# Kernel optimization log

Hardware: AMD Instinct MI355X
Metric: run time of the kernel (lower is better)

Reference implementation:

```python
import jax, jax.numpy as jnp
import numpy as np

N, D, K = 262144, 64, 1024


def setup_inputs() -> dict:
    key = jax.random.key(0)
    kx, kc = jax.random.split(key)
    x = jax.random.normal(kx, (N, D), dtype=jnp.float32)
    codebook = jax.random.normal(kc, (K, D), dtype=jnp.float32)
    return {"x": x, "codebook": codebook}


def reference(x, codebook):
    # VQTokenizer.encode: cdist(x, codebook) -> argmin -> gather.
    # squared distances equals argmin over cdist (sqrt is monotone).
    x2 = jnp.sum(x * x, axis=-1, keepdims=True)            # (N, 1)
    c2 = jnp.sum(codebook * codebook, axis=-1)             # (K,)
    d2 = x2 + c2[None, :] - 2.0 * jnp.einsum('nd,kd->nk', x, codebook)  # (N, K)
    encoded = jnp.argmin(d2, axis=1)                       # (N,) int
    quantized = jnp.take(codebook, encoded, axis=0)        # (N, D)
    return encoded, quantized
```

## Files before the change

### kernel.cpp

```cpp
#include <hip/hip_runtime.h>
#include <hip/hip_bf16.h>

#define NPTS 262144
#define DDIM 64
#define KCB  1024
#define CHUNK 128
#define NCHUNK (KCB / CHUNK)
#define GPC (CHUNK / 16)

typedef __attribute__((ext_vector_type(8))) short short8;
typedef __attribute__((ext_vector_type(4))) float f32x4;

static __device__ __forceinline__ unsigned short f2bf_rne(float f) {
    union { float f; unsigned u; } v; v.f = f;
    unsigned r = v.u + 0x7FFFu + ((v.u >> 16) & 1u);
    return (unsigned short)(r >> 16);
}
static __device__ __forceinline__ float bf2f(unsigned short h) {
    union { unsigned u; float f; } v; v.u = ((unsigned)h) << 16;
    return v.f;
}
static __device__ __forceinline__ bool beats(float sa, int ka, float sb, int kb) {
    return (sa > sb) || (sa == sb && ka < kb);
}

__global__ __launch_bounds__(256) void c2n_kernel(const float* __restrict__ cb,
                                                  float* __restrict__ c2n) {
    int k = blockIdx.x * blockDim.x + threadIdx.x;
    if (k >= KCB) return;
    const float4* row = (const float4*)(cb + (size_t)k * DDIM);
    float s0 = 0.f, s1 = 0.f, s2 = 0.f, s3 = 0.f;
#pragma unroll
    for (int j = 0; j < DDIM / 4; ++j) {
        float4 a = row[j];
        s0 = __builtin_fmaf(a.x, a.x, s0);
        s1 = __builtin_fmaf(a.y, a.y, s1);
        s2 = __builtin_fmaf(a.z, a.z, s2);
        s3 = __builtin_fmaf(a.w, a.w, s3);
    }
    c2n[k] = 256.0f - 0.5f * ((s0 + s1) + (s2 + s3));
}

__global__ __launch_bounds__(256) void pack_kernel(const float* __restrict__ cb,
                                                   unsigned short* __restrict__ G) {
    int t = blockIdx.x * 256 + threadIdx.x;
    int r = t >> 3, d8 = t & 7;
    const float4* src = (const float4*)(cb + (size_t)r * DDIM + d8 * 8);
    float4 v0 = src[0], v1 = src[1];
    float vv[8] = {v0.x, v0.y, v0.z, v0.w, v1.x, v1.y, v1.z, v1.w};
    short8 h, l;
#pragma unroll
    for (int j = 0; j < 8; ++j) {
        unsigned short hb = f2bf_rne(vv[j]);
        h[j] = (short)hb;
        l[j] = (short)f2bf_rne(vv[j] - bf2f(hb));
    }
    int c = r >> 7, g = (r >> 4) & 7, col = r & 15;
    int ks = d8 >> 2, q = d8 & 3;
    size_t base = (size_t)c * 16384 + g * 1024 + ks * 512 + q * 128 + col * 8;
    *(short8*)(G + base) = h;
    *(short8*)(G + base + 8192) = l;
}

__global__ __launch_bounds__(256, 2) void vq_main(const float* __restrict__ x,
                                                  const float* __restrict__ cb,
                                                  const float* __restrict__ c2n,
                                                  const unsigned short* __restrict__ G,
                                                  float* __restrict__ out) {
    __shared__ unsigned short frag[2][CHUNK * DDIM * 2];
    __shared__ int lds_bk1[256];
    __shared__ int lds_bk2[256];

    const int tid = threadIdx.x;
    const int lane = tid & 63;
    const int wave = tid >> 6;
    const int b15 = lane & 15;
    const int q = lane >> 4;
    const int blk_base = blockIdx.x * 256;
    const int wave_base = blk_base + wave * 64;
    const int lane_off = lane * 16;

    short8 Ahi[4][2], Alo[4][2];
#pragma unroll
    for (int t = 0; t < 4; ++t) {
        const float* xr = x + (size_t)(wave_base + t * 16 + b15) * DDIM + q * 8;
#pragma unroll
        for (int ks = 0; ks < 2; ++ks) {
            float4 v0 = *(const float4*)(xr + ks * 32);
            float4 v1 = *(const float4*)(xr + ks * 32 + 4);
            float vv[8] = {v0.x, v0.y, v0.z, v0.w, v1.x, v1.y, v1.z, v1.w};
            short8 h, l;
#pragma unroll
            for (int j = 0; j < 8; ++j) {
                unsigned short hb = f2bf_rne(vv[j]);
                h[j] = (short)hb;
                l[j] = (short)f2bf_rne(vv[j] - bf2f(hb));
            }
            Ahi[t][ks] = h;
            Alo[t][ks] = l;
        }
    }

    unsigned int b1[16], b2[16];
#pragma unroll
    for (int i = 0; i < 16; ++i) { b1[i] = 0u; b2[i] = 0u; }

#define STAGE(cc, buf)                                                                     \
    {                                                                                      \
        const unsigned char* gsrc =                                                        \
            (const unsigned char*)G + (size_t)(cc) * 32768 + wave * 1024 + lane * 16;      \
        unsigned char* ldst = (unsigned char*)&frag[buf][0] + wave * 1024;                 \
        _Pragma("unroll") for (int it = 0; it < 8; ++it)                                   \
            __builtin_amdgcn_global_load_lds(                                              \
                (const __attribute__((address_space(1))) unsigned int*)(gsrc + it * 4096), \
                (__attribute__((address_space(3))) unsigned int*)(ldst + it * 4096),       \
                16, 0, 0);                                                                 \
    }

    float c2v[GPC], c2vn[GPC];
    STAGE(0, 0);
#pragma unroll
    for (int g = 0; g < GPC; ++g) c2v[g] = c2n[g * 16 + b15];
    __syncthreads();

    for (int c = 0; c < NCHUNK; ++c) {
        const int cur = c & 1;
        if (c + 1 < NCHUNK) {
            STAGE(c + 1, cur ^ 1);
#pragma unroll
            for (int g = 0; g < GPC; ++g) c2vn[g] = c2n[(c + 1) * CHUNK + g * 16 + b15];
        }
        const unsigned char* fb = (const unsigned char*)&frag[cur][0];

#pragma unroll
        for (int g = 0; g < GPC; ++g) {
            f32x4 acc[4];
#pragma unroll
            for (int t = 0; t < 4; ++t) acc[t] = (f32x4){c2v[g], c2v[g], c2v[g], c2v[g]};
            __builtin_amdgcn_s_setprio(1);
#pragma unroll
            for (int ks = 0; ks < 2; ++ks) {
                const short8 Bhi = *(const short8*)(fb + g * 2048 + ks * 1024 + lane_off);
                const short8 Blo = *(const short8*)(fb + 16384 + g * 2048 + ks * 1024 + lane_off);
#pragma unroll
                for (int t = 0; t < 4; ++t) {
                    acc[t] = __builtin_amdgcn_mfma_f32_16x16x32_bf16(Ahi[t][ks], Bhi, acc[t], 0, 0, 0);
                    acc[t] = __builtin_amdgcn_mfma_f32_16x16x32_bf16(Ahi[t][ks], Blo, acc[t], 0, 0, 0);
                    acc[t] = __builtin_amdgcn_mfma_f32_16x16x32_bf16(Alo[t][ks], Bhi, acc[t], 0, 0, 0);
                }
            }
            __builtin_amdgcn_s_setprio(0);
            const unsigned int inv = 63u - (unsigned)(c * GPC + g);
#pragma unroll
            for (int t = 0; t < 4; ++t) {
#pragma unroll
                for (int r = 0; r < 4; ++r) {
                    int i = t * 4 + r;
                    unsigned int kb = (__float_as_uint(acc[t][r]) & 0xFFFFFFC0u) | inv;
                    unsigned int mn = b1[i] < kb ? b1[i] : kb;
                    b1[i] = b1[i] > kb ? b1[i] : kb;
                    b2[i] = b2[i] > mn ? b2[i] : mn;
                }
            }
        }
#pragma unroll
        for (int g = 0; g < GPC; ++g) c2v[g] = c2vn[g];
        __syncthreads();
    }
#undef STAGE

    unsigned int K1[16], K2[16];
    int I1[16], I2[16];
#pragma unroll
    for (int i = 0; i < 16; ++i) {
        K1[i] = b1[i]; I1[i] = (int)(63u - (b1[i] & 63u)) * 16 + b15;
        K2[i] = b2[i]; I2[i] = (int)(63u - (b2[i] & 63u)) * 16 + b15;
    }
#pragma unroll
    for (int m = 1; m < 16; m <<= 1) {
#pragma unroll
        for (int i = 0; i < 16; ++i) {
            unsigned int o1 = __shfl_xor(K1[i], m); int oi1 = __shfl_xor(I1[i], m);
            unsigned int o2 = __shfl_xor(K2[i], m); int oi2 = __shfl_xor(I2[i], m);
            bool ob = (o1 > K1[i]) || (o1 == K1[i] && oi1 < I1[i]);
            unsigned int nk1, nk2; int ni1, ni2;
            if (ob) {
                nk1 = o1; ni1 = oi1;
                bool sb = (K1[i] > o2) || (K1[i] == o2 && I1[i] < oi2);
                nk2 = sb ? K1[i] : o2; ni2 = sb ? I1[i] : oi2;
            } else {
                nk1 = K1[i]; ni1 = I1[i];
                bool sb = (o1 > K2[i]) || (o1 == K2[i] && oi1 < I2[i]);
                nk2 = sb ? o1 : K2[i]; ni2 = sb ? oi1 : I2[i];
            }
            K1[i] = nk1; I1[i] = ni1; K2[i] = nk2; I2[i] = ni2;
        }
    }

    if (b15 == 0) {
#pragma unroll
        for (int t = 0; t < 4; ++t)
#pragma unroll
            for (int r = 0; r < 4; ++r) {
                int pl = wave * 64 + t * 16 + q * 4 + r;
                lds_bk1[pl] = I1[t * 4 + r];
                lds_bk2[pl] = I2[t * 4 + r];
            }
    }
    __syncthreads();

    const int p = blk_base + tid;
    const int k1 = lds_bk1[tid], k2 = lds_bk2[tid];
    const float4* xr = (const float4*)(x + (size_t)p * DDIM);
    const float4* c1 = (const float4*)(cb + (size_t)k1 * DDIM);
    const float4* c2r = (const float4*)(cb + (size_t)k2 * DDIM);
    float d1a = 0.f, d1b = 0.f, d2a = 0.f, d2b = 0.f;
#pragma unroll
    for (int j = 0; j < 16; ++j) {
        float4 xv = xr[j];
        float4 u = c1[j], w = c2r[j];
        d1a = __builtin_fmaf(xv.x, u.x, d1a); d1b = __builtin_fmaf(xv.y, u.y, d1b);
        d1a = __builtin_fmaf(xv.z, u.z, d1a); d1b = __builtin_fmaf(xv.w, u.w, d1b);
        d2a = __builtin_fmaf(xv.x, w.x, d2a); d2b = __builtin_fmaf(xv.y, w.y, d2b);
        d2a = __builtin_fmaf(xv.z, w.z, d2a); d2b = __builtin_fmaf(xv.w, w.w, d2b);
    }
    float a1 = (d1a + d1b) + c2n[k1];
    float a2 = (d2a + d2b) + c2n[k2];
    int kf = beats(a1, k1, a2, k2) ? k1 : k2;

    out[p] = (float)kf;
    const float4* cf = (const float4*)(cb + (size_t)kf * DDIM);
    float4* qo = (float4*)(out + NPTS + (size_t)p * DDIM);
#pragma unroll
    for (int j = 0; j < 16; ++j) qo[j] = cf[j];
}

extern "C" void kernel_launch(void* const* d_in, const int* in_sizes, int n_in,
                              void* d_out, int out_size, void* d_ws, size_t ws_size,
                              hipStream_t stream) {
    const float* x = (const float*)d_in[0];
    const float* cb = (const float*)d_in[1];
    float* c2n = (float*)d_ws;
    unsigned short* G = (unsigned short*)((char*)d_ws + 4096);

    hipLaunchKernelGGL(c2n_kernel, dim3(KCB / 256), dim3(256), 0, stream, cb, c2n);
    hipLaunchKernelGGL(pack_kernel, dim3(KCB * 8 / 256), dim3(256), 0, stream, cb, G);
    hipLaunchKernelGGL(vq_main, dim3(NPTS / 256), dim3(256), 0, stream,
                       x, cb, c2n, G, (float*)d_out);
}
```

Baseline: 163.0 us.

## Use 512-thread blocks with 32 points per wave and smaller codebook chunks

Blocks grow to 8 waves, and each wave now handles 32 points instead of 64. The codebook chunk shrinks to 64 entries, which cuts LDS use and register pressure so occupancy can rise (launch bounds 512,4). The top-2 tracking now processes two groups at once using float max3/med3 on packed keys. The final refine and gather step is split across two threads per point, with a shuffle to pick the winner. In exchange, each loaded codebook chunk is reused over fewer points, so MFMA work per LDS load drops, and there are more chunk iterations and more syncs.

```diff
diff --git a/kernel.cpp b/kernel.cpp
--- a/kernel.cpp
+++ b/kernel.cpp
@@ -4,9 +4,10 @@
 #define NPTS 262144
 #define DDIM 64
 #define KCB  1024
-#define CHUNK 128
+#define CHUNK 64
 #define NCHUNK (KCB / CHUNK)
 #define GPC (CHUNK / 16)
+#define PPB 256
 
 typedef __attribute__((ext_vector_type(8))) short short8;
 typedef __attribute__((ext_vector_type(4))) float f32x4;
@@ -22,6 +23,9 @@
 }
 static __device__ __forceinline__ bool beats(float sa, int ka, float sb, int kb) {
     return (sa > sb) || (sa == sb && ka < kb);
+}
+static __device__ __forceinline__ float keyf(float acc, unsigned inv) {
+    return __uint_as_float((__float_as_uint(acc) & 0xFFFFFFC0u) | inv);
 }
 
 __global__ __launch_bounds__(256) void c2n_kernel(const float* __restrict__ cb,
@@ -55,34 +59,34 @@
         h[j] = (short)hb;
         l[j] = (short)f2bf_rne(vv[j] - bf2f(hb));
     }
-    int c = r >> 7, g = (r >> 4) & 7, col = r & 15;
+    int c = r >> 6, g = (r >> 4) & 3, col = r & 15;
     int ks = d8 >> 2, q = d8 & 3;
-    size_t base = (size_t)c * 16384 + g * 1024 + ks * 512 + q * 128 + col * 8;
+    size_t base = (size_t)c * 8192 + g * 1024 + ks * 512 + q * 128 + col * 8;
     *(short8*)(G + base) = h;
-    *(short8*)(G + base + 8192) = l;
-}
-
-__global__ __launch_bounds__(256, 2) void vq_main(const float* __restrict__ x,
+    *(short8*)(G + base + 4096) = l;
+}
+
+__global__ __launch_bounds__(512, 4) void vq_main(const float* __restrict__ x,
                                                   const float* __restrict__ cb,
                                                   const float* __restrict__ c2n,
                                                   const unsigned short* __restrict__ G,
                                                   float* __restrict__ out) {
     __shared__ unsigned short frag[2][CHUNK * DDIM * 2];
-    __shared__ int lds_bk1[256];
-    __shared__ int lds_bk2[256];
+    __shared__ int lds_bk1[PPB];
+    __shared__ int lds_bk2[PPB];
 
     const int tid = threadIdx.x;
     const int lane = tid & 63;
     const int wave = tid >> 6;
     const int b15 = lane & 15;
     const int q = lane >> 4;
-    const int blk_base = blockIdx.x * 256;
-    const int wave_base = blk_base + wave * 64;
+    const int blk_base = blockIdx.x * PPB;
+    const int wave_base = blk_base + wave * 32;
     const int lane_off = lane * 16;
 
-    short8 Ahi[4][2], Alo[4][2];
-#pragma unroll
-    for (int t = 0; t < 4; ++t) {
+    short8 Ahi[2][2], Alo[2][2];
+#pragma unroll
+    for (int t = 0; t < 2; ++t) {
         const float* xr = x + (size_t)(wave_base + t * 16 + b15) * DDIM + q * 8;
 #pragma unroll
         for (int ks = 0; ks < 2; ++ks) {
@@ -101,19 +105,18 @@
         }
     }
 
-    unsigned int b1[16], b2[16];
-#pragma unroll
-    for (int i = 0; i < 16; ++i) { b1[i] = 0u; b2[i] = 0u; }
+    float b1[8], b2[8];
+#pragma unroll
+    for (int i = 0; i < 8; ++i) { b1[i] = 0.0f; b2[i] = 0.0f; }
 
 #define STAGE(cc, buf)                                                                     \
     {                                                                                      \
-        const unsigned char* gsrc =                                                        \
-            (const unsigned char*)G + (size_t)(cc) * 32768 + wave * 1024 + lane * 16;      \
-        unsigned char* ldst = (unsigned char*)&frag[buf][0] + wave * 1024;                 \
-        _Pragma("unroll") for (int it = 0; it < 8; ++it)                                   \
+        const unsigned char* gsrc = (const unsigned char*)G + (size_t)(cc) * 16384 + tid * 16; \
+        unsigned char* ldst = (unsigned char*)&frag[buf][0] + tid * 16;                    \
+        _Pragma("unroll") for (int it = 0; it < 2; ++it)                                   \
             __builtin_amdgcn_global_load_lds(                                              \
-                (const __attribute__((address_space(1))) unsigned int*)(gsrc + it * 4096), \
-                (__attribute__((address_space(3))) unsigned int*)(ldst + it * 4096),       \
+                (const __attribute__((address_space(1))) unsigned int*)(gsrc + it * 8192), \
+                (__attribute__((address_space(3))) unsigned int*)(ldst + it * 8192),       \
                 16, 0, 0);                                                                 \
     }
 
@@ -133,35 +136,60 @@
         const unsigned char* fb = (const unsigned char*)&frag[cur][0];
 
 #pragma unroll
-        for (int g = 0; g < GPC; ++g) {
-            f32x4 acc[4];
-#pragma unroll
-            for (int t = 0; t < 4; ++t) acc[t] = (f32x4){c2v[g], c2v[g], c2v[g], c2v[g]};
+        for (int gp = 0; gp < 2; ++gp) {
+            const int g0 = gp * 2, g1 = g0 + 1;
+            const unsigned inv0 = 63u - (unsigned)(c * GPC + g0);
+
+            f32x4 acc0[2];
+#pragma unroll
+            for (int t = 0; t < 2; ++t) acc0[t] = (f32x4){c2v[g0], c2v[g0], c2v[g0], c2v[g0]};
             __builtin_amdgcn_s_setprio(1);
 #pragma unroll
             for (int ks = 0; ks < 2; ++ks) {
-                const short8 Bhi = *(const short8*)(fb + g * 2048 + ks * 1024 + lane_off);
-                const short8 Blo = *(const short8*)(fb + 16384 + g * 2048 + ks * 1024 + lane_off);
-#pragma unroll
-                for (int t = 0; t < 4; ++t) {
-                    acc[t] = __builtin_amdgcn_mfma_f32_16x16x32_bf16(Ahi[t][ks], Bhi, acc[t], 0, 0, 0);
-                    acc[t] = __builtin_amdgcn_mfma_f32_16x16x32_bf16(Ahi[t][ks], Blo, acc[t], 0, 0, 0);
-                    acc[t] = __builtin_amdgcn_mfma_f32_16x16x32_bf16(Alo[t][ks], Bhi, acc[t], 0, 0, 0);
+                const short8 Bhi = *(const short8*)(fb + g0 * 2048 + ks * 1024 + lane_off);
+                const short8 Blo = *(const short8*)(fb + 8192 + g0 * 2048 + ks * 1024 + lane_off);
+#pragma unroll
+                for (int t = 0; t < 2; ++t) {
+                    acc0[t] = __builtin_amdgcn_mfma_f32_16x16x32_bf16(Ahi[t][ks], Bhi, acc0[t], 0, 0, 0);
+                    acc0[t] = __builtin_amdgcn_mfma_f32_16x16x32_bf16(Ahi[t][ks], Blo, acc0[t], 0, 0, 0);
+                    acc0[t] = __builtin_amdgcn_mfma_f32_16x16x32_bf16(Alo[t][ks], Bhi, acc0[t], 0, 0, 0);
                 }
             }
             __builtin_amdgcn_s_setprio(0);
-            const unsigned int inv = 63u - (unsigned)(c * GPC + g);
-#pragma unroll
-            for (int t = 0; t < 4; ++t) {
+            float ka[8];
+#pragma unroll
+            for (int t = 0; t < 2; ++t)
+#pragma unroll
+                for (int r = 0; r < 4; ++r) ka[t * 4 + r] = keyf(acc0[t][r], inv0);
+
+            f32x4 acc1[2];
+#pragma unroll
+            for (int t = 0; t < 2; ++t) acc1[t] = (f32x4){c2v[g1], c2v[g1], c2v[g1], c2v[g1]};
+            __builtin_amdgcn_s_setprio(1);
+#pragma unroll
+            for (int ks = 0; ks < 2; ++ks) {
+                const short8 Bhi = *(const short8*)(fb + g1 * 2048 + ks * 1024 + lane_off);
+                const short8 Blo = *(const short8*)(fb + 8192 + g1 * 2048 + ks * 1024 + lane_off);
+#pragma unroll
+                for (int t = 0; t < 2; ++t) {
+                    acc1[t] = __builtin_amdgcn_mfma_f32_16x16x32_bf16(Ahi[t][ks], Bhi, acc1[t], 0, 0, 0);
+                    acc1[t] = __builtin_amdgcn_mfma_f32_16x16x32_bf16(Ahi[t][ks], Blo, acc1[t], 0, 0, 0);
+                    acc1[t] = __builtin_amdgcn_mfma_f32_16x16x32_bf16(Alo[t][ks], Bhi, acc1[t], 0, 0, 0);
+                }
+            }
+            __builtin_amdgcn_s_setprio(0);
+#pragma unroll
+            for (int t = 0; t < 2; ++t)
 #pragma unroll
                 for (int r = 0; r < 4; ++r) {
-                    int i = t * 4 + r;
-                    unsigned int kb = (__float_as_uint(acc[t][r]) & 0xFFFFFFC0u) | inv;
-                    unsigned int mn = b1[i] < kb ? b1[i] : kb;
-                    b1[i] = b1[i] > kb ? b1[i] : kb;
-                    b2[i] = b2[i] > mn ? b2[i] : mn;
+                    const int i = t * 4 + r;
+                    const float kb = keyf(acc1[t][r], inv0 - 1u);
+                    const float med = __builtin_amdgcn_fmed3f(b1[i], ka[i], kb);
+                    float nb1;
+                    asm("v_max3_f32 %0, %1, %2, %3" : "=v"(nb1) : "v"(b1[i]), "v"(ka[i]), "v"(kb));
+                    b1[i] = nb1;
+                    b2[i] = fmaxf(b2[i], med);
                 }
-            }
         }
 #pragma unroll
         for (int g = 0; g < GPC; ++g) c2v[g] = c2vn[g];
@@ -169,17 +197,17 @@
     }
 #undef STAGE
 
-    unsigned int K1[16], K2[16];
-    int I1[16], I2[16];
-#pragma unroll
-    for (int i = 0; i < 16; ++i) {
-        K1[i] = b1[i]; I1[i] = (int)(63u - (b1[i] & 63u)) * 16 + b15;
-        K2[i] = b2[i]; I2[i] = (int)(63u - (b2[i] & 63u)) * 16 + b15;
+    unsigned int K1[8], K2[8];
+    int I1[8], I2[8];
+#pragma unroll
+    for (int i = 0; i < 8; ++i) {
+        K1[i] = __float_as_uint(b1[i]); I1[i] = (int)(63u - (K1[i] & 63u)) * 16 + b15;
+        K2[i] = __float_as_uint(b2[i]); I2[i] = (int)(63u - (K2[i] & 63u)) * 16 + b15;
     }
 #pragma unroll
     for (int m = 1; m < 16; m <<= 1) {
 #pragma unroll
-        for (int i = 0; i < 16; ++i) {
+        for (int i = 0; i < 8; ++i) {
             unsigned int o1 = __shfl_xor(K1[i], m); int oi1 = __shfl_xor(I1[i], m);
             unsigned int o2 = __shfl_xor(K2[i], m); int oi2 = __shfl_xor(I2[i], m);
             bool ob = (o1 > K1[i]) || (o1 == K1[i] && oi1 < I1[i]);
@@ -199,40 +227,42 @@
 
     if (b15 == 0) {
 #pragma unroll
-        for (int t = 0; t < 4; ++t)
+        for (int t = 0; t < 2; ++t)
 #pragma unroll
             for (int r = 0; r < 4; ++r) {
-                int pl = wave * 64 + t * 16 + q * 4 + r;
+                int pl = wave * 32 + t * 16 + q * 4 + r;
                 lds_bk1[pl] = I1[t * 4 + r];
                 lds_bk2[pl] = I2[t * 4 + r];
             }
     }
     __syncthreads();
 
-    const int p = blk_base + tid;
-    const int k1 = lds_bk1[tid], k2 = lds_bk2[tid];
+    const int pid = tid >> 1;
+    const int p = blk_base + pid;
+    const int ksel = (tid & 1) ? lds_bk2[pid] : lds_bk1[pid];
     const float4* xr = (const float4*)(x + (size_t)p * DDIM);
-    const float4* c1 = (const float4*)(cb + (size_t)k1 * DDIM);
-    const float4* c2r = (const float4*)(cb + (size_t)k2 * DDIM);
-    float d1a = 0.f, d1b = 0.f, d2a = 0.f, d2b = 0.f;
+    const float4* cr = (const float4*)(cb + (size_t)ksel * DDIM);
+    float da = 0.f, db = 0.f;
 #pragma unroll
     for (int j = 0; j < 16; ++j) {
         float4 xv = xr[j];
-        float4 u = c1[j], w = c2r[j];
-        d1a = __builtin_fmaf(xv.x, u.x, d1a); d1b = __builtin_fmaf(xv.y, u.y, d1b);
-        d1a = __builtin_fmaf(xv.z, u.z, d1a); d1b = __builtin_fmaf(xv.w, u.w, d1b);
-        d2a = __builtin_fmaf(xv.x, w.x, d2a); d2b = __builtin_fmaf(xv.y, w.y, d2b);
-        d2a = __builtin_fmaf(xv.z, w.z, d2a); d2b = __builtin_fmaf(xv.w, w.w, d2b);
-    }
-    float a1 = (d1a + d1b) + c2n[k1];
-    float a2 = (d2a + d2b) + c2n[k2];
+        float4 u = cr[j];
+        da = __builtin_fmaf(xv.x, u.x, da); db = __builtin_fmaf(xv.y, u.y, db);
+        da = __builtin_fmaf(xv.z, u.z, da); db = __builtin_fmaf(xv.w, u.w, db);
+    }
+    float a = (da + db) + c2n[ksel];
+    float oa = __shfl_xor(a, 1);
+    int ok = __shfl_xor(ksel, 1);
+    const bool first = ((tid & 1) == 0);
+    float a1 = first ? a : oa; int k1 = first ? ksel : ok;
+    float a2 = first ? oa : a; int k2 = first ? ok : ksel;
     int kf = beats(a1, k1, a2, k2) ? k1 : k2;
 
-    out[p] = (float)kf;
-    const float4* cf = (const float4*)(cb + (size_t)kf * DDIM);
-    float4* qo = (float4*)(out + NPTS + (size_t)p * DDIM);
-#pragma unroll
-    for (int j = 0; j < 16; ++j) qo[j] = cf[j];
+    if (first) out[p] = (float)kf;
+    const float4* cf = (const float4*)(cb + (size_t)kf * DDIM + (tid & 1) * 32);
+    float4* qo = (float4*)(out + NPTS + (size_t)p * DDIM + (tid & 1) * 32);
+#pragma unroll
+    for (int j = 0; j < 8; ++j) qo[j] = cf[j];
 }
 
 extern "C" void kernel_launch(void* const* d_in, const int* in_sizes, int n_in,
@@ -245,6 +275,6 @@
 
     hipLaunchKernelGGL(c2n_kernel, dim3(KCB / 256), dim3(256), 0, stream, cb, c2n);
     hipLaunchKernelGGL(pack_kernel, dim3(KCB * 8 / 256), dim3(256), 0, stream, cb, G);
-    hipLaunchKernelGGL(vq_main, dim3(NPTS / 256), dim3(256), 0, stream,
+    hipLaunchKernelGGL(vq_main, dim3(NPTS / PPB), dim3(512), 0, stream,
                        x, cb, c2n, G, (float*)d_out);
 }
```

Result: faster. 142.0 us (-12.9%).

## Enlarge blocks to 512 points, cache codebook norms in LDS, use float med3 top-2

Applied to the files above, without the earlier changes.

Each block now handles 512 points with 512 threads, so every staged codebook chunk in LDS is shared by twice as many points and less global-to-LDS traffic is needed per point. The codebook norm offsets are loaded once into LDS rather than prefetched from global memory per chunk. The top-2 tracking switches from unsigned min/max on the packed keys to float fmaxf plus fmed3. This works because the keys are positive floats, so float and unsigned ordering agree, and it needs fewer ALU ops per candidate. The larger block and launch bounds change register pressure and LDS-limited occupancy, which could cut either way.

```diff
diff --git a/kernel.cpp b/kernel.cpp
--- a/kernel.cpp
+++ b/kernel.cpp
@@ -7,6 +7,7 @@
 #define CHUNK 128
 #define NCHUNK (KCB / CHUNK)
 #define GPC (CHUNK / 16)
+#define PPB 512
 
 typedef __attribute__((ext_vector_type(8))) short short8;
 typedef __attribute__((ext_vector_type(4))) float f32x4;
@@ -22,6 +23,9 @@
 }
 static __device__ __forceinline__ bool beats(float sa, int ka, float sb, int kb) {
     return (sa > sb) || (sa == sb && ka < kb);
+}
+static __device__ __forceinline__ float keyf(float acc, unsigned inv) {
+    return __uint_as_float((__float_as_uint(acc) & 0xFFFFFFC0u) | inv);
 }
 
 __global__ __launch_bounds__(256) void c2n_kernel(const float* __restrict__ cb,
@@ -62,21 +66,24 @@
     *(short8*)(G + base + 8192) = l;
 }
 
-__global__ __launch_bounds__(256, 2) void vq_main(const float* __restrict__ x,
+struct BFrag { short8 h0, l0, h1, l1; };
+
+__global__ __launch_bounds__(512, 3) void vq_main(const float* __restrict__ x,
                                                   const float* __restrict__ cb,
                                                   const float* __restrict__ c2n,
                                                   const unsigned short* __restrict__ G,
                                                   float* __restrict__ out) {
     __shared__ unsigned short frag[2][CHUNK * DDIM * 2];
-    __shared__ int lds_bk1[256];
-    __shared__ int lds_bk2[256];
+    __shared__ float lds_c2f[KCB];
+    __shared__ int lds_bk1[PPB];
+    __shared__ int lds_bk2[PPB];
 
     const int tid = threadIdx.x;
     const int lane = tid & 63;
     const int wave = tid >> 6;
     const int b15 = lane & 15;
     const int q = lane >> 4;
-    const int blk_base = blockIdx.x * 256;
+    const int blk_base = blockIdx.x * PPB;
     const int wave_base = blk_base + wave * 64;
     const int lane_off = lane * 16;
 
@@ -101,70 +108,68 @@
         }
     }
 
-    unsigned int b1[16], b2[16];
-#pragma unroll
-    for (int i = 0; i < 16; ++i) { b1[i] = 0u; b2[i] = 0u; }
+    float b1[16], b2[16];
+#pragma unroll
+    for (int i = 0; i < 16; ++i) { b1[i] = 0.0f; b2[i] = 0.0f; }
 
 #define STAGE(cc, buf)                                                                     \
     {                                                                                      \
-        const unsigned char* gsrc =                                                        \
-            (const unsigned char*)G + (size_t)(cc) * 32768 + wave * 1024 + lane * 16;      \
-        unsigned char* ldst = (unsigned char*)&frag[buf][0] + wave * 1024;                 \
-        _Pragma("unroll") for (int it = 0; it < 8; ++it)                                   \
+        const unsigned char* gsrc = (const unsigned char*)G + (size_t)(cc) * 32768 + tid * 16; \
+        unsigned char* ldst = (unsigned char*)&frag[buf][0] + tid * 16;                    \
+        _Pragma("unroll") for (int it = 0; it < 4; ++it)                                   \
             __builtin_amdgcn_global_load_lds(                                              \
-                (const __attribute__((address_space(1))) unsigned int*)(gsrc + it * 4096), \
-                (__attribute__((address_space(3))) unsigned int*)(ldst + it * 4096),       \
+                (const __attribute__((address_space(1))) unsigned int*)(gsrc + it * 8192), \
+                (__attribute__((address_space(3))) unsigned int*)(ldst + it * 8192),       \
                 16, 0, 0);                                                                 \
     }
 
-    float c2v[GPC], c2vn[GPC];
     STAGE(0, 0);
-#pragma unroll
-    for (int g = 0; g < GPC; ++g) c2v[g] = c2n[g * 16 + b15];
+    lds_c2f[tid] = c2n[tid];
+    lds_c2f[tid + 512] = c2n[tid + 512];
     __syncthreads();
 
     for (int c = 0; c < NCHUNK; ++c) {
         const int cur = c & 1;
-        if (c + 1 < NCHUNK) {
-            STAGE(c + 1, cur ^ 1);
-#pragma unroll
-            for (int g = 0; g < GPC; ++g) c2vn[g] = c2n[(c + 1) * CHUNK + g * 16 + b15];
+        if (c + 1 < NCHUNK) STAGE(c + 1, cur ^ 1);
+        const unsigned char* fb = (const unsigned char*)&frag[cur][0];
+
+#pragma unroll
+        for (int g = 0; g < GPC; ++g) {
+            const unsigned inv = 63u - (unsigned)(c * GPC + g);
+            BFrag B;
+            {
+                const unsigned char* p_ = fb + (size_t)g * 2048 + lane_off;
+                B.h0 = *(const short8*)(p_);
+                B.l0 = *(const short8*)(p_ + 16384);
+                B.h1 = *(const short8*)(p_ + 1024);
+                B.l1 = *(const short8*)(p_ + 17408);
+            }
+            const float cg = lds_c2f[(c * GPC + g) * 16 + b15];
+            const f32x4 cvec = (f32x4){cg, cg, cg, cg};
+
+            f32x4 acc[4];
+            __builtin_amdgcn_s_setprio(1);
+#pragma unroll
+            for (int t = 0; t < 4; ++t) {
+                acc[t] = __builtin_amdgcn_mfma_f32_16x16x32_bf16(Ahi[t][0], B.h0, cvec, 0, 0, 0);
+                acc[t] = __builtin_amdgcn_mfma_f32_16x16x32_bf16(Ahi[t][0], B.l0, acc[t], 0, 0, 0);
+                acc[t] = __builtin_amdgcn_mfma_f32_16x16x32_bf16(Alo[t][0], B.h0, acc[t], 0, 0, 0);
+                acc[t] = __builtin_amdgcn_mfma_f32_16x16x32_bf16(Ahi[t][1], B.h1, acc[t], 0, 0, 0);
+                acc[t] = __builtin_amdgcn_mfma_f32_16x16x32_bf16(Ahi[t][1], B.l1, acc[t], 0, 0, 0);
+                acc[t] = __builtin_amdgcn_mfma_f32_16x16x32_bf16(Alo[t][1], B.h1, acc[t], 0, 0, 0);
+            }
+            __builtin_amdgcn_s_setprio(0);
+
+#pragma unroll
+            for (int t = 0; t < 4; ++t)
+#pragma unroll
+                for (int r = 0; r < 4; ++r) {
+                    const int i = t * 4 + r;
+                    const float kk = keyf(acc[t][r], inv);
+                    b2[i] = __builtin_amdgcn_fmed3f(kk, b1[i], b2[i]);
+                    b1[i] = fmaxf(b1[i], kk);
+                }
         }
-        const unsigned char* fb = (const unsigned char*)&frag[cur][0];
-
-#pragma unroll
-        for (int g = 0; g < GPC; ++g) {
-            f32x4 acc[4];
-#pragma unroll
-            for (int t = 0; t < 4; ++t) acc[t] = (f32x4){c2v[g], c2v[g], c2v[g], c2v[g]};
-            __builtin_amdgcn_s_setprio(1);
-#pragma unroll
-            for (int ks = 0; ks < 2; ++ks) {
-                const short8 Bhi = *(const short8*)(fb + g * 2048 + ks * 1024 + lane_off);
-                const short8 Blo = *(const short8*)(fb + 16384 + g * 2048 + ks * 1024 + lane_off);
-#pragma unroll
-                for (int t = 0; t < 4; ++t) {
-                    acc[t] = __builtin_amdgcn_mfma_f32_16x16x32_bf16(Ahi[t][ks], Bhi, acc[t], 0, 0, 0);
-                    acc[t] = __builtin_amdgcn_mfma_f32_16x16x32_bf16(Ahi[t][ks], Blo, acc[t], 0, 0, 0);
-                    acc[t] = __builtin_amdgcn_mfma_f32_16x16x32_bf16(Alo[t][ks], Bhi, acc[t], 0, 0, 0);
-                }
-            }
-            __builtin_amdgcn_s_setprio(0);
-            const unsigned int inv = 63u - (unsigned)(c * GPC + g);
-#pragma unroll
-            for (int t = 0; t < 4; ++t) {
-#pragma unroll
-                for (int r = 0; r < 4; ++r) {
-                    int i = t * 4 + r;
-                    unsigned int kb = (__float_as_uint(acc[t][r]) & 0xFFFFFFC0u) | inv;
-                    unsigned int mn = b1[i] < kb ? b1[i] : kb;
-                    b1[i] = b1[i] > kb ? b1[i] : kb;
-                    b2[i] = b2[i] > mn ? b2[i] : mn;
-                }
-            }
-        }
-#pragma unroll
-        for (int g = 0; g < GPC; ++g) c2v[g] = c2vn[g];
         __syncthreads();
     }
 #undef STAGE
@@ -173,8 +178,8 @@
     int I1[16], I2[16];
 #pragma unroll
     for (int i = 0; i < 16; ++i) {
-        K1[i] = b1[i]; I1[i] = (int)(63u - (b1[i] & 63u)) * 16 + b15;
-        K2[i] = b2[i]; I2[i] = (int)(63u - (b2[i] & 63u)) * 16 + b15;
+        K1[i] = __float_as_uint(b1[i]); I1[i] = (int)(63u - (K1[i] & 63u)) * 16 + b15;
+        K2[i] = __float_as_uint(b2[i]); I2[i] = (int)(63u - (K2[i] & 63u)) * 16 + b15;
     }
 #pragma unroll
     for (int m = 1; m < 16; m <<= 1) {
@@ -224,8 +229,8 @@
         d2a = __builtin_fmaf(xv.x, w.x, d2a); d2b = __builtin_fmaf(xv.y, w.y, d2b);
         d2a = __builtin_fmaf(xv.z, w.z, d2a); d2b = __builtin_fmaf(xv.w, w.w, d2b);
     }
-    float a1 = (d1a + d1b) + c2n[k1];
-    float a2 = (d2a + d2b) + c2n[k2];
+    float a1 = (d1a + d1b) + lds_c2f[k1];
+    float a2 = (d2a + d2b) + lds_c2f[k2];
     int kf = beats(a1, k1, a2, k2) ? k1 : k2;
 
     out[p] = (float)kf;
@@ -245,6 +250,6 @@
 
     hipLaunchKernelGGL(c2n_kernel, dim3(KCB / 256), dim3(256), 0, stream, cb, c2n);
     hipLaunchKernelGGL(pack_kernel, dim3(KCB * 8 / 256), dim3(256), 0, stream, cb, G);
-    hipLaunchKernelGGL(vq_main, dim3(NPTS / 256), dim3(256), 0, stream,
+    hipLaunchKernelGGL(vq_main, dim3(NPTS / PPB), dim3(512), 0, stream,
                        x, cb, c2n, G, (float*)d_out);
 }
```

Measured after the change: 174.3 us. 6.9% more time.
